# Kernel tuning notes

Measured on AMD Instinct MI355X. Metric: run time of the kernel, lower is better.

Reference implementation:

```python
import jax, jax.numpy as jnp
import numpy as np


def setup_inputs() -> dict:
    key = jax.random.key(0)
    k1, k2, k3, k4 = jax.random.split(key, 4)
    B, S, D = 8, 2048, 1024
    x = jax.random.normal(k1, (B, S, D), dtype=jnp.float32)
    scale = 1.0 / np.sqrt(D)  # glorot-ish magnitude
    Wq = jax.random.normal(k2, (D, D), dtype=jnp.float32) * scale
    Wk = jax.random.normal(k3, (D, D), dtype=jnp.float32) * scale
    Wv = jax.random.normal(k4, (D, D), dtype=jnp.float32) * scale
    return {"x": x, "Wq": Wq, "Wk": Wk, "Wv": Wv}


def reference(x, Wq, Wk, Wv):
    # q,k,v: [B,S,D]
    q = jnp.einsum("bsd,de->bse", x, Wq)
    k = jnp.einsum("bsd,de->bse", x, Wk)
    v = jnp.einsum("bsd,de->bse", x, Wv)
    d = k.shape[-1]
    # scores: [B,S,S], scaled by sqrt(d)
    scores = jnp.einsum("bqd,bkd->bqk", q, k) / jnp.sqrt(jnp.asarray(d, x.dtype))
    attn = jax.nn.softmax(scores, axis=-1)
    out = jnp.einsum("bqk,bkd->bqd", attn, v)
    return out
```

## Files before the change

kernel.cpp:

```cpp
#include <hip/hip_runtime.h>
#include <hip/hip_bf16.h>

typedef __bf16 bf16x8 __attribute__((ext_vector_type(8)));
typedef float  f32x4  __attribute__((ext_vector_type(4)));

static __device__ __forceinline__ unsigned short f2bf(float f) {
  unsigned int u = __float_as_uint(f);
  u += 0x7FFFu + ((u >> 16) & 1u);
  return (unsigned short)(u >> 16);
}

static __device__ __forceinline__ void gl_lds16(const void* g, void* l) {
  __builtin_amdgcn_global_load_lds(
      (const __attribute__((address_space(1))) void*)g,
      (__attribute__((address_space(3))) void*)l,
      16, 0, 0);
}

__global__ __launch_bounds__(256) void cast_f32_bf16(
    const float* __restrict__ in, unsigned short* __restrict__ out, int n) {
  int i = (blockIdx.x * 256 + threadIdx.x) * 4;
  const int stride = gridDim.x * 256 * 4;
  for (; i < n; i += stride) {
    float4 f = *(const float4*)(in + i);
    ushort4 o;
    o.x = f2bf(f.x); o.y = f2bf(f.y); o.z = f2bf(f.z); o.w = f2bf(f.w);
    *(ushort4*)(out + i) = o;
  }
}

__global__ __launch_bounds__(256) void transpose_cast_w(
    const float* __restrict__ w, unsigned short* __restrict__ wt) {
  __shared__ float tile[16][17];
  const int tx = threadIdx.x & 15, ty = threadIdx.x >> 4;
  const int bx = blockIdx.x * 16, by = blockIdx.y * 16;
  tile[ty][tx] = w[(size_t)(by + ty) * 1024 + bx + tx];
  __syncthreads();
  wt[(size_t)(bx + ty) * 1024 + by + tx] = f2bf(tile[tx][ty]);
}

template <int MODE>
__global__ __launch_bounds__(256, 2) void gemm_bt(
    const unsigned short* __restrict__ A, int lda, size_t astride,
    const unsigned short* __restrict__ B, int ldb, size_t bstride,
    int K, void* __restrict__ Cv, int ldc, size_t cstride,
    float* __restrict__ aux) {
  __shared__ __align__(16) unsigned char lds[49152];
  const unsigned d2 = blockIdx.x + gridDim.x * blockIdx.y;
  const unsigned ty = d2 % gridDim.y;
  const unsigned tx = d2 / gridDim.y;
  const int bn0 = tx * 128;
  const int bm0 = ty * 128;
  A += (size_t)blockIdx.z * astride;
  B += (size_t)blockIdx.z * bstride;

  const int tid = threadIdx.x;
  const int wid = tid >> 6, lane = tid & 63;
  const int wr = wid >> 1, wc = wid & 1;
  const int l15 = lane & 15, kq = lane >> 4;

  const int e0 = wid * 512 + lane * 8;
  const int r0 = e0 >> 5, c0 = e0 & 31;
  const size_t aoff0 = (size_t)(bm0 + r0) * lda + c0;
  const size_t aoff1 = (size_t)(bm0 + r0 + 64) * lda + c0;
  const size_t boff0 = (size_t)(bn0 + r0) * ldb + c0;
  const size_t boff1 = (size_t)(bn0 + r0 + 64) * ldb + c0;

#define STAGE(t) do { \
    unsigned char* s_ = lds + ((t) % 3) * 16384 + wid * 1024; \
    const int kc_ = (t) << 5; \
    gl_lds16(A + aoff0 + kc_, s_); \
    gl_lds16(A + aoff1 + kc_, s_ + 4096); \
    gl_lds16(B + boff0 + kc_, s_ + 8192); \
    gl_lds16(B + boff1 + kc_, s_ + 12288); \
  } while (0)
#define DSR(dst, addr) asm volatile("ds_read_b128 %0, %1" : "=v"(dst) : "v"(addr))

  const unsigned ldsbase =
      (unsigned)(unsigned long long)(__attribute__((address_space(3))) unsigned char*)lds;
  const unsigned aA = ldsbase + (wr * 64 + l15) * 64 + kq * 16;
  const unsigned aB = ldsbase + 8192 + (wc * 64 + l15) * 64 + kq * 16;

  f32x4 acc[4][4] = {};
  const int nkt = K >> 5;

  STAGE(0);
  STAGE(1);

  for (int t = 0; t < nkt; ++t) {
    if (t < nkt - 1) asm volatile("s_waitcnt vmcnt(4)" ::: "memory");
    else             asm volatile("s_waitcnt vmcnt(0)" ::: "memory");
    __builtin_amdgcn_s_barrier();

    const unsigned so = (unsigned)(t % 3) * 16384u;
    bf16x8 af[4], bg[4];
#pragma unroll
    for (int mi = 0; mi < 4; ++mi) DSR(af[mi], so + aA + mi * 1024);
#pragma unroll
    for (int ni = 0; ni < 4; ++ni) DSR(bg[ni], so + aB + ni * 1024);

    if (t + 2 < nkt) STAGE(t + 2);

    asm volatile("s_waitcnt lgkmcnt(0)" ::: "memory");
    __builtin_amdgcn_sched_barrier(0);
    __builtin_amdgcn_s_setprio(1);
#pragma unroll
    for (int mi = 0; mi < 4; ++mi)
#pragma unroll
      for (int ni = 0; ni < 4; ++ni)
        acc[mi][ni] = __builtin_amdgcn_mfma_f32_16x16x32_bf16(af[mi], bg[ni], acc[mi][ni], 0, 0, 0);
    __builtin_amdgcn_s_setprio(0);
  }
#undef STAGE
#undef DSR

  if constexpr (MODE == 3) {
#pragma unroll
    for (int mi = 0; mi < 4; ++mi)
#pragma unroll
      for (int ni = 0; ni < 4; ++ni)
#pragma unroll
        for (int r = 0; r < 4; ++r) {
          const int row = bm0 + wr * 64 + mi * 16 + kq * 4 + r;
          const int col = bn0 + wc * 64 + ni * 16 + l15;
          const float v = acc[mi][ni][r];
          unsigned short* q = (unsigned short*)Cv;
          if (col < 1024) {
            q[(size_t)row * 1024 + col] = f2bf(v);
          } else if (col < 2048) {
            q[16777216u + (size_t)row * 1024 + (col - 1024)] = f2bf(v);
          } else {
            const int b = row >> 11, s = row & 2047;
            q[33554432u + ((size_t)(b * 1024 + (col - 2048))) * 2048 + s] = f2bf(v);
          }
        }
  } else if constexpr (MODE == 4) {
    __shared__ float redsm[128][2];
    unsigned short* pp = (unsigned short*)Cv + (size_t)blockIdx.z * cstride;
    float rs[4][4];
#pragma unroll
    for (int mi = 0; mi < 4; ++mi)
#pragma unroll
      for (int r = 0; r < 4; ++r) rs[mi][r] = 0.f;
#pragma unroll
    for (int mi = 0; mi < 4; ++mi)
#pragma unroll
      for (int ni = 0; ni < 4; ++ni)
#pragma unroll
        for (int r = 0; r < 4; ++r) {
          const float e = exp2f(acc[mi][ni][r] * 0.045084220027780106f);
          rs[mi][r] += e;
          const int row = bm0 + wr * 64 + mi * 16 + kq * 4 + r;
          const int col = bn0 + wc * 64 + ni * 16 + l15;
          pp[(size_t)row * ldc + col] = f2bf(e);
        }
#pragma unroll
    for (int mi = 0; mi < 4; ++mi)
#pragma unroll
      for (int r = 0; r < 4; ++r) {
        float s = rs[mi][r];
        s += __shfl_xor(s, 1); s += __shfl_xor(s, 2);
        s += __shfl_xor(s, 4); s += __shfl_xor(s, 8);
        rs[mi][r] = s;
      }
    if (l15 == 0) {
#pragma unroll
      for (int mi = 0; mi < 4; ++mi)
#pragma unroll
        for (int r = 0; r < 4; ++r)
          redsm[wr * 64 + mi * 16 + kq * 4 + r][wc] = rs[mi][r];
    }
    __syncthreads();
    if (tid < 128)
      aux[((size_t)blockIdx.z * 16 + tx) * 2048 + bm0 + tid] =
          redsm[tid][0] + redsm[tid][1];
  } else {
    const float* inv = aux + (size_t)blockIdx.z * 2048;
    float* op = (float*)Cv + (size_t)blockIdx.z * cstride;
#pragma unroll
    for (int mi = 0; mi < 4; ++mi)
#pragma unroll
      for (int r = 0; r < 4; ++r) {
        const int row = bm0 + wr * 64 + mi * 16 + kq * 4 + r;
        const float iv = inv[row];
#pragma unroll
        for (int ni = 0; ni < 4; ++ni) {
          const int col = bn0 + wc * 64 + ni * 16 + l15;
          op[(size_t)row * ldc + col] = acc[mi][ni][r] * iv;
        }
      }
  }
}

__global__ __launch_bounds__(256) void combine_inv(
    const float* __restrict__ part, float* __restrict__ inv, int n) {
  const int i = blockIdx.x * 256 + threadIdx.x;
  if (i >= n) return;
  const int z = i >> 11, row = i & 2047;
  const float* p = part + ((size_t)z * 16) * 2048 + row;
  float s = 0.f;
#pragma unroll
  for (int j = 0; j < 16; ++j) s += p[j * 2048];
  inv[i] = 1.0f / s;
}

extern "C" void kernel_launch(void* const* d_in, const int* in_sizes, int n_in,
                              void* d_out, int out_size, void* d_ws, size_t ws_size,
                              hipStream_t stream) {
  const float* x  = (const float*)d_in[0];
  const float* Wq = (const float*)d_in[1];
  const float* Wk = (const float*)d_in[2];
  const float* Wv = (const float*)d_in[3];
  float* out = (float*)d_out;
  char* ws = (char*)d_ws;

  unsigned short* xb     = (unsigned short*)ws;
  unsigned short* wt_all = (unsigned short*)(ws + 33554432);
  unsigned short* qb     = (unsigned short*)(ws + 39845888);
  unsigned short* kb     = qb + 16777216;
  unsigned short* vt     = kb + 16777216;
  const size_t off_scores = 140509184ull;

  const size_t per_b = 8388608ull + 131072ull + 8192ull;
  int G; char *pPc, *partc, *invc;
  const size_t avail = ws_size > off_scores ? ws_size - off_scores : 0;
  G = (int)(avail / per_b); if (G > 8) G = 8;
  if (G >= 1) {
    pPc   = ws + off_scores;
    partc = pPc + (size_t)G * 8388608ull;
    invc  = partc + (size_t)G * 131072ull;
  } else {
    G = 2;
    pPc   = ws;
    partc = ws + 2 * 8388608ull;
    invc  = partc + 2 * 131072ull;
  }

  cast_f32_bf16<<<2048, 256, 0, stream>>>(x, xb, 16384 * 1024);
  transpose_cast_w<<<dim3(64, 64), 256, 0, stream>>>(Wq, wt_all);
  transpose_cast_w<<<dim3(64, 64), 256, 0, stream>>>(Wk, wt_all + 1048576);
  transpose_cast_w<<<dim3(64, 64), 256, 0, stream>>>(Wv, wt_all + 2097152);

  gemm_bt<3><<<dim3(24, 128), 256, 0, stream>>>(xb, 1024, 0, wt_all, 1024, 0,
                                                1024, qb, 0, 0, nullptr);

  for (int b0 = 0; b0 < 8; b0 += G) {
    const int g = (8 - b0) < G ? (8 - b0) : G;
    const size_t so = (size_t)b0 * 2097152;
    gemm_bt<4><<<dim3(16, 16, g), 256, 0, stream>>>(
        qb + so, 1024, 2097152, kb + so, 1024, 2097152, 1024,
        (unsigned short*)pPc, 2048, 4194304, (float*)partc);
    combine_inv<<<(g * 2048 + 255) / 256, 256, 0, stream>>>(
        (const float*)partc, (float*)invc, g * 2048);
    gemm_bt<5><<<dim3(8, 16, g), 256, 0, stream>>>(
        (const unsigned short*)pPc, 2048, 4194304,
        vt + so, 2048, 2097152, 2048,
        out + so, 1024, 2097152, (float*)invc);
  }
}
```

Before: 363.5 us.

## Switch GEMM to double-buffered LDS and fuse softmax-inverse into PV GEMM

Reduces the GEMM LDS ring from three stages to two, issuing the next tile load before computing the current one and synchronizing at the end of each iteration. The separate combine_inv kernel is removed: the PV GEMM now sums the partial row sums and computes reciprocals into shared memory itself. The three weight transpose launches are merged into one launch over a z-dimension. The shorter prefetch distance may expose more global-load latency in exchange for lower LDS use and fewer launches.

```diff
diff --git a/kernel.cpp b/kernel.cpp
--- a/kernel.cpp
+++ b/kernel.cpp
@@ -29,14 +29,17 @@
   }
 }
 
-__global__ __launch_bounds__(256) void transpose_cast_w(
-    const float* __restrict__ w, unsigned short* __restrict__ wt) {
+__global__ __launch_bounds__(256) void transpose_cast_w3(
+    const float* __restrict__ w0, const float* __restrict__ w1,
+    const float* __restrict__ w2, unsigned short* __restrict__ wt) {
   __shared__ float tile[16][17];
+  const float* w = blockIdx.z == 0 ? w0 : (blockIdx.z == 1 ? w1 : w2);
+  unsigned short* o = wt + (size_t)blockIdx.z * 1048576;
   const int tx = threadIdx.x & 15, ty = threadIdx.x >> 4;
   const int bx = blockIdx.x * 16, by = blockIdx.y * 16;
   tile[ty][tx] = w[(size_t)(by + ty) * 1024 + bx + tx];
   __syncthreads();
-  wt[(size_t)(bx + ty) * 1024 + by + tx] = f2bf(tile[tx][ty]);
+  o[(size_t)(bx + ty) * 1024 + by + tx] = f2bf(tile[tx][ty]);
 }
 
 template <int MODE>
@@ -45,7 +48,8 @@
     const unsigned short* __restrict__ B, int ldb, size_t bstride,
     int K, void* __restrict__ Cv, int ldc, size_t cstride,
     float* __restrict__ aux) {
-  __shared__ __align__(16) unsigned char lds[49152];
+  __shared__ __align__(16) unsigned char lds[32768];
+  __shared__ float smInv[128];
   const unsigned d2 = blockIdx.x + gridDim.x * blockIdx.y;
   const unsigned ty = d2 % gridDim.y;
   const unsigned tx = d2 / gridDim.y;
@@ -59,6 +63,16 @@
   const int wr = wid >> 1, wc = wid & 1;
   const int l15 = lane & 15, kq = lane >> 4;
 
+  if constexpr (MODE == 5) {
+    if (tid < 128) {
+      const float* p = aux + (size_t)blockIdx.z * 32768 + bm0 + tid;
+      float s = 0.f;
+#pragma unroll
+      for (int j = 0; j < 16; ++j) s += p[j * 2048];
+      smInv[tid] = 1.0f / s;
+    }
+  }
+
   const int e0 = wid * 512 + lane * 8;
   const int r0 = e0 >> 5, c0 = e0 & 31;
   const size_t aoff0 = (size_t)(bm0 + r0) * lda + c0;
@@ -67,7 +81,7 @@
   const size_t boff1 = (size_t)(bn0 + r0 + 64) * ldb + c0;
 
 #define STAGE(t) do { \
-    unsigned char* s_ = lds + ((t) % 3) * 16384 + wid * 1024; \
+    unsigned char* s_ = lds + ((t) & 1) * 16384 + wid * 1024; \
     const int kc_ = (t) << 5; \
     gl_lds16(A + aoff0 + kc_, s_); \
     gl_lds16(A + aoff1 + kc_, s_ + 4096); \
@@ -85,22 +99,18 @@
   const int nkt = K >> 5;
 
   STAGE(0);
-  STAGE(1);
+  asm volatile("s_waitcnt vmcnt(0)" ::: "memory");
+  __builtin_amdgcn_s_barrier();
 
   for (int t = 0; t < nkt; ++t) {
-    if (t < nkt - 1) asm volatile("s_waitcnt vmcnt(4)" ::: "memory");
-    else             asm volatile("s_waitcnt vmcnt(0)" ::: "memory");
-    __builtin_amdgcn_s_barrier();
-
-    const unsigned so = (unsigned)(t % 3) * 16384u;
+    if (t + 1 < nkt) STAGE(t + 1);
+    const unsigned bofs = (unsigned)(t & 1) * 16384u;
+
     bf16x8 af[4], bg[4];
 #pragma unroll
-    for (int mi = 0; mi < 4; ++mi) DSR(af[mi], so + aA + mi * 1024);
-#pragma unroll
-    for (int ni = 0; ni < 4; ++ni) DSR(bg[ni], so + aB + ni * 1024);
-
-    if (t + 2 < nkt) STAGE(t + 2);
-
+    for (int mi = 0; mi < 4; ++mi) DSR(af[mi], bofs + aA + mi * 1024);
+#pragma unroll
+    for (int ni = 0; ni < 4; ++ni) DSR(bg[ni], bofs + aB + ni * 1024);
     asm volatile("s_waitcnt lgkmcnt(0)" ::: "memory");
     __builtin_amdgcn_sched_barrier(0);
     __builtin_amdgcn_s_setprio(1);
@@ -110,6 +120,8 @@
       for (int ni = 0; ni < 4; ++ni)
         acc[mi][ni] = __builtin_amdgcn_mfma_f32_16x16x32_bf16(af[mi], bg[ni], acc[mi][ni], 0, 0, 0);
     __builtin_amdgcn_s_setprio(0);
+    asm volatile("s_waitcnt vmcnt(0)" ::: "memory");
+    __builtin_amdgcn_s_barrier();
   }
 #undef STAGE
 #undef DSR
@@ -175,14 +187,13 @@
       aux[((size_t)blockIdx.z * 16 + tx) * 2048 + bm0 + tid] =
           redsm[tid][0] + redsm[tid][1];
   } else {
-    const float* inv = aux + (size_t)blockIdx.z * 2048;
     float* op = (float*)Cv + (size_t)blockIdx.z * cstride;
 #pragma unroll
     for (int mi = 0; mi < 4; ++mi)
 #pragma unroll
       for (int r = 0; r < 4; ++r) {
         const int row = bm0 + wr * 64 + mi * 16 + kq * 4 + r;
-        const float iv = inv[row];
+        const float iv = smInv[wr * 64 + mi * 16 + kq * 4 + r];
 #pragma unroll
         for (int ni = 0; ni < 4; ++ni) {
           const int col = bn0 + wc * 64 + ni * 16 + l15;
@@ -190,18 +201,6 @@
         }
       }
   }
-}
-
-__global__ __launch_bounds__(256) void combine_inv(
-    const float* __restrict__ part, float* __restrict__ inv, int n) {
-  const int i = blockIdx.x * 256 + threadIdx.x;
-  if (i >= n) return;
-  const int z = i >> 11, row = i & 2047;
-  const float* p = part + ((size_t)z * 16) * 2048 + row;
-  float s = 0.f;
-#pragma unroll
-  for (int j = 0; j < 16; ++j) s += p[j * 2048];
-  inv[i] = 1.0f / s;
 }
 
 extern "C" void kernel_launch(void* const* d_in, const int* in_sizes, int n_in,
@@ -221,25 +220,21 @@
   unsigned short* vt     = kb + 16777216;
   const size_t off_scores = 140509184ull;
 
-  const size_t per_b = 8388608ull + 131072ull + 8192ull;
-  int G; char *pPc, *partc, *invc;
+  const size_t per_b = 8388608ull + 131072ull;
+  int G; char *pPc, *partc;
   const size_t avail = ws_size > off_scores ? ws_size - off_scores : 0;
   G = (int)(avail / per_b); if (G > 8) G = 8;
   if (G >= 1) {
     pPc   = ws + off_scores;
     partc = pPc + (size_t)G * 8388608ull;
-    invc  = partc + (size_t)G * 131072ull;
   } else {
     G = 2;
     pPc   = ws;
     partc = ws + 2 * 8388608ull;
-    invc  = partc + 2 * 131072ull;
   }
 
   cast_f32_bf16<<<2048, 256, 0, stream>>>(x, xb, 16384 * 1024);
-  transpose_cast_w<<<dim3(64, 64), 256, 0, stream>>>(Wq, wt_all);
-  transpose_cast_w<<<dim3(64, 64), 256, 0, stream>>>(Wk, wt_all + 1048576);
-  transpose_cast_w<<<dim3(64, 64), 256, 0, stream>>>(Wv, wt_all + 2097152);
+  transpose_cast_w3<<<dim3(64, 64, 3), 256, 0, stream>>>(Wq, Wk, Wv, wt_all);
 
   gemm_bt<3><<<dim3(24, 128), 256, 0, stream>>>(xb, 1024, 0, wt_all, 1024, 0,
                                                 1024, qb, 0, 0, nullptr);
@@ -250,11 +245,9 @@
     gemm_bt<4><<<dim3(16, 16, g), 256, 0, stream>>>(
         qb + so, 1024, 2097152, kb + so, 1024, 2097152, 1024,
         (unsigned short*)pPc, 2048, 4194304, (float*)partc);
-    combine_inv<<<(g * 2048 + 255) / 256, 256, 0, stream>>>(
-        (const float*)partc, (float*)invc, g * 2048);
     gemm_bt<5><<<dim3(8, 16, g), 256, 0, stream>>>(
         (const unsigned short*)pPc, 2048, 4194304,
         vt + so, 2048, 2097152, 2048,
-        out + so, 1024, 2097152, (float*)invc);
-  }
-}
+        out + so, 1024, 2097152, (float*)partc);
+  }
+}
```

Result: no change. 361.6 us (-0.5%).
